# Optimization experiments

Measured on AMD Instinct MI355X. Metric: run time of the kernel, lower is better.

## Reference

```python
import jax, jax.numpy as jnp
import numpy as np

INPUT, HIDDEN, OUTPUT = 512, 1024, 512
B, T = 64, 512


def setup_inputs() -> dict:
    key = jax.random.key(0)
    ks = jax.random.split(key, 10)
    s_ih = (2.0 / (INPUT + HIDDEN)) ** 0.5
    s_hh = (2.0 / (INPUT + HIDDEN)) ** 0.5
    s_hy = (2.0 / (HIDDEN + OUTPUT)) ** 0.5
    inp = {
        "x": jax.random.normal(ks[0], (B, T, INPUT), dtype=jnp.float32),
        "W_xi": jax.random.normal(ks[1], (INPUT, HIDDEN), dtype=jnp.float32) * s_ih,
        "W_hi": jax.random.normal(ks[2], (HIDDEN, HIDDEN), dtype=jnp.float32) * s_hh,
        "b_i": jnp.zeros((HIDDEN,), dtype=jnp.float32),
        "W_xf": jax.random.normal(ks[3], (INPUT, HIDDEN), dtype=jnp.float32) * s_ih,
        "W_hf": jax.random.normal(ks[4], (HIDDEN, HIDDEN), dtype=jnp.float32) * s_hh,
        "b_f": jnp.zeros((HIDDEN,), dtype=jnp.float32),
        "W_xo": jax.random.normal(ks[5], (INPUT, HIDDEN), dtype=jnp.float32) * s_ih,
        "W_ho": jax.random.normal(ks[6], (HIDDEN, HIDDEN), dtype=jnp.float32) * s_hh,
        "b_o": jnp.zeros((HIDDEN,), dtype=jnp.float32),
        "W_xc": jax.random.normal(ks[7], (INPUT, HIDDEN), dtype=jnp.float32) * s_ih,
        "W_hc": jax.random.normal(ks[8], (HIDDEN, HIDDEN), dtype=jnp.float32) * s_hh,
        "b_c": jnp.zeros((HIDDEN,), dtype=jnp.float32),
        "W_hy": jax.random.normal(ks[9], (HIDDEN, OUTPUT), dtype=jnp.float32) * s_hy,
        "b_y": jnp.zeros((OUTPUT,), dtype=jnp.float32),
    }
    return inp


def reference(x, W_xi, W_hi, b_i, W_xf, W_hf, b_f, W_xo, W_ho, b_o,
              W_xc, W_hc, b_c, W_hy, b_y):
    Bn, Tn, _ = x.shape
    H = W_hi.shape[0]
    # Precompute input projections for all timesteps (one big GEMM per gate).
    xi = jnp.einsum('bti,ih->bth', x, W_xi) + b_i  # [B,T,H]
    xf = jnp.einsum('bti,ih->bth', x, W_xf) + b_f
    xo = jnp.einsum('bti,ih->bth', x, W_xo) + b_o
    xc = jnp.einsum('bti,ih->bth', x, W_xc) + b_c
    # time-major for scan
    xs = (jnp.swapaxes(xi, 0, 1), jnp.swapaxes(xf, 0, 1),
          jnp.swapaxes(xo, 0, 1), jnp.swapaxes(xc, 0, 1))

    def step(carry, xt):
        h, c = carry
        xi_t, xf_t, xo_t, xc_t = xt
        i_t = jax.nn.sigmoid(xi_t + h @ W_hi)
        f_t = jax.nn.sigmoid(xf_t + h @ W_hf)
        o_t = jax.nn.sigmoid(xo_t + h @ W_ho)
        cand = jnp.tanh(xc_t + h @ W_hc)
        c = f_t * c + i_t * cand
        h = o_t * jnp.tanh(c)
        return (h, c), h

    h0 = jnp.zeros((Bn, H), dtype=x.dtype)
    c0 = jnp.zeros((Bn, H), dtype=x.dtype)
    _, hs = jax.lax.scan(step, (h0, c0), xs)  # hs: [T,B,H]
    # Output projection applied to every step's hidden state.
    ys = jnp.einsum('tbh,ho->tbo', hs, W_hy) + b_y
    return jnp.swapaxes(ys, 0, 1)  # [B,T,O]
```

## Files before the change

### kernel.cpp

```cpp
#include <hip/hip_runtime.h>
#include <hip/hip_bf16.h>
#include <cstdint>

#define B_   64
#define T_   512
#define IN_  512
#define H_   1024
#define O_   512
#define NG   4096
#define KC   1536
#define BT   32768
#define BH   65536
#define NWG  128

using bs8 = __attribute__((ext_vector_type(8))) short;
using f4  = __attribute__((ext_vector_type(4))) float;

__device__ __forceinline__ ushort f2bf(float f) {
    union { float f; uint32_t u; } v; v.f = f;
    uint32_t r = v.u + 0x7fffu + ((v.u >> 16) & 1u);
    return (ushort)(r >> 16);
}
__device__ __forceinline__ float sigm(float x) { return 1.f / (1.f + __expf(-x)); }
__device__ __forceinline__ float tanh_(float x) {
    x = fminf(fmaxf(x, -15.f), 15.f);
    float e = __expf(2.f * x);
    return (e - 1.f) / (e + 1.f);
}
__device__ __forceinline__ void coh_store16(void* p, f4 v) {
    asm volatile("global_store_dwordx4 %0, %1, off sc0 sc1" :: "v"(p), "v"(v) : "memory");
}


__global__ void k_pack_x(const float* __restrict__ x, ushort* __restrict__ xP) {
    const int n8 = BT * IN_ / 8;
    for (int i = blockIdx.x * blockDim.x + threadIdx.x; i < n8; i += gridDim.x * blockDim.x) {
        const int e8 = i & 3, b = (i >> 2) & 63, kk = (i >> 8) & 15, t = i >> 12;
        const float* s = x + ((size_t)b * T_ + t) * IN_ + kk * 32 + e8 * 8;
        f4 v0 = *reinterpret_cast<const f4*>(s);
        f4 v1 = *reinterpret_cast<const f4*>(s + 4);
        uint4 q;
        q.x = (uint32_t)f2bf(v0[0]) | ((uint32_t)f2bf(v0[1]) << 16);
        q.y = (uint32_t)f2bf(v0[2]) | ((uint32_t)f2bf(v0[3]) << 16);
        q.z = (uint32_t)f2bf(v1[0]) | ((uint32_t)f2bf(v1[1]) << 16);
        q.w = (uint32_t)f2bf(v1[2]) | ((uint32_t)f2bf(v1[3]) << 16);
        *reinterpret_cast<uint4*>(xP + ((size_t)t * 16 + kk) * 2048 + b * 32 + e8 * 8) = q;
    }
}

__global__ void k_build_wcT(const float* __restrict__ xi, const float* __restrict__ xf,
                            const float* __restrict__ xo, const float* __restrict__ xc,
                            const float* __restrict__ hi, const float* __restrict__ hf,
                            const float* __restrict__ ho, const float* __restrict__ hc,
                            ushort* __restrict__ dst) {
    const int total = NG * KC;
    for (int i = blockIdx.x * blockDim.x + threadIdx.x; i < total; i += gridDim.x * blockDim.x) {
        int n = i / KC, k = i - n * KC;
        int g = n & 3, h = n >> 2;
        float v;
        if (k < IN_) {
            const float* s = (g == 0) ? xi : ((g == 1) ? xf : ((g == 2) ? xo : xc));
            v = s[(size_t)k * H_ + h];
        } else {
            const float* s = (g == 0) ? hi : ((g == 1) ? hf : ((g == 2) ? ho : hc));
            v = s[(size_t)(k - IN_) * H_ + h];
        }
        dst[i] = f2bf(v);
    }
}

__global__ void k_build_whyT(const float* __restrict__ w, ushort* __restrict__ dst) {
    const int total = O_ * H_;
    for (int i = blockIdx.x * blockDim.x + threadIdx.x; i < total; i += gridDim.x * blockDim.x) {
        int o = i >> 10, k = i & (H_ - 1);
        dst[i] = f2bf(w[(size_t)k * O_ + o]);
    }
}

__global__ void k_build_bias(const float* __restrict__ bi, const float* __restrict__ bff,
                             const float* __restrict__ bo, const float* __restrict__ bc,
                             float* __restrict__ dst) {
    int i = blockIdx.x * blockDim.x + threadIdx.x;
    if (i < NG) {
        int g = i & 3, h = i >> 2;
        dst[i] = (g == 0) ? bi[h] : ((g == 1) ? bff[h] : ((g == 2) ? bo[h] : bc[h]));
    }
}

#define WROWB 3072
#define WSWZ(row, kbyte) ((row) * WROWB + ((kbyte) ^ (((row) & 7) << 4)))

__global__ void __launch_bounds__(256, 1)
k_persist(const ushort* __restrict__ WcT, const ushort* __restrict__ xP,
          ushort* __restrict__ hs, float* __restrict__ cst,
          const float* __restrict__ biasc, uint32_t* __restrict__ flags,
          int t0, int nsteps) {
    __shared__ ushort Wl[32 * 1536];
    __shared__ ushort hout[64][8];
    const int g = blockIdx.x, tid = threadIdx.x;
    const int lane = tid & 63, w = tid >> 6;
    const int n0 = g * 32;
    const int l15 = lane & 15, lq = lane >> 4;

    {
        char* p = (char*)Wl;
        for (int i = tid; i < 32 * 192; i += 256) {
            const int row = i / 192, c8 = i - row * 192;
            bs8 v = *reinterpret_cast<const bs8*>(WcT + (size_t)(n0 + row) * KC + c8 * 8);
            *reinterpret_cast<bs8*>(p + WSWZ(row, c8 * 16)) = v;
        }
    }
    const char* wl = (const char*)Wl;

    const int bmy = w * 16 + l15;
    const int u0 = g * 8;
    const f4 bia0 = *reinterpret_cast<const f4*>(biasc + n0 + lq * 4);
    const f4 bia1 = *reinterpret_cast<const f4*>(biasc + n0 + 16 + lq * 4);
    float c0 = 0.f, c1 = 0.f;
    if (t0 != 0) {
        c0 = cst[(size_t)bmy * H_ + u0 + lq];
        c1 = cst[(size_t)bmy * H_ + u0 + 4 + lq];
    }
    const ushort* xbase = xP + (size_t)t0 * 32768 + (size_t)bmy * 32 + lq * 8;
    const ushort* hrd   = hs + (size_t)bmy * 32 + lq * 8;
    __syncthreads();

    bs8 xv[16];
#pragma unroll
    for (int kk = 0; kk < 16; ++kk)
        xv[kk] = *reinterpret_cast<const bs8*>(xbase + kk * 2048);

    for (int s = 0; s < nsteps; ++s) {
        const ushort* hb = hrd + (size_t)s * BH;
        bs8 hv0[16], hv1[16];
#pragma unroll
        for (int kk = 0; kk < 16; ++kk)
            hv0[kk] = *reinterpret_cast<const bs8*>(hb + kk * 2048);

        f4 a0 = {0.f, 0.f, 0.f, 0.f}, a1 = {0.f, 0.f, 0.f, 0.f};
#pragma unroll
        for (int kk = 0; kk < 16; ++kk) {
            bs8 wa0 = *reinterpret_cast<const bs8*>(wl + WSWZ(l15,      kk * 64 + lq * 16));
            bs8 wa1 = *reinterpret_cast<const bs8*>(wl + WSWZ(16 + l15, kk * 64 + lq * 16));
            a0 = __builtin_amdgcn_mfma_f32_16x16x32_bf16(wa0, xv[kk], a0, 0, 0, 0);
            a1 = __builtin_amdgcn_mfma_f32_16x16x32_bf16(wa1, xv[kk], a1, 0, 0, 0);
        }
#pragma unroll
        for (int kk = 0; kk < 16; ++kk)
            hv1[kk] = *reinterpret_cast<const bs8*>(hb + (16 + kk) * 2048);
#pragma unroll
        for (int kk = 0; kk < 16; ++kk) {
            bs8 wa0 = *reinterpret_cast<const bs8*>(wl + WSWZ(l15,      1024 + kk * 64 + lq * 16));
            bs8 wa1 = *reinterpret_cast<const bs8*>(wl + WSWZ(16 + l15, 1024 + kk * 64 + lq * 16));
            a0 = __builtin_amdgcn_mfma_f32_16x16x32_bf16(wa0, hv0[kk], a0, 0, 0, 0);
            a1 = __builtin_amdgcn_mfma_f32_16x16x32_bf16(wa1, hv0[kk], a1, 0, 0, 0);
        }
#pragma unroll
        for (int kk = 0; kk < 16; ++kk) {
            bs8 wa0 = *reinterpret_cast<const bs8*>(wl + WSWZ(l15,      2048 + kk * 64 + lq * 16));
            bs8 wa1 = *reinterpret_cast<const bs8*>(wl + WSWZ(16 + l15, 2048 + kk * 64 + lq * 16));
            a0 = __builtin_amdgcn_mfma_f32_16x16x32_bf16(wa0, hv1[kk], a0, 0, 0, 0);
            a1 = __builtin_amdgcn_mfma_f32_16x16x32_bf16(wa1, hv1[kk], a1, 0, 0, 0);
        }

        {
            float pi = a0[0] + bia0[0], pf = a0[1] + bia0[1];
            float po = a0[2] + bia0[2], pc = a0[3] + bia0[3];
            float iv = sigm(pi), fv = sigm(pf), ov = sigm(po), cv = tanh_(pc);
            c0 = fv * c0 + iv * cv;
            hout[bmy][lq] = f2bf(ov * tanh_(c0));
        }
        {
            float pi = a1[0] + bia1[0], pf = a1[1] + bia1[1];
            float po = a1[2] + bia1[2], pc = a1[3] + bia1[3];
            float iv = sigm(pi), fv = sigm(pf), ov = sigm(po), cv = tanh_(pc);
            c1 = fv * c1 + iv * cv;
            hout[bmy][4 + lq] = f2bf(ov * tanh_(c1));
        }
        __syncthreads();

        if (w == 0) {
            f4 hv = *reinterpret_cast<f4*>(&hout[lane][0]);
            ushort* dst = hs + (size_t)(s + 1) * BH + (size_t)(g >> 2) * 2048
                        + (size_t)lane * 32 + (g & 3) * 8;
            coh_store16(dst, hv);
            asm volatile("s_waitcnt vmcnt(0)" ::: "memory");
            if (tid == 0)
                __hip_atomic_store(&flags[g], (uint32_t)(s + 1),
                                   __ATOMIC_RELAXED, __HIP_MEMORY_SCOPE_AGENT);
        }

        if (s + 1 < nsteps) {
#pragma unroll
            for (int kk = 0; kk < 16; ++kk)
                xv[kk] = *reinterpret_cast<const bs8*>(xbase + (size_t)(s + 1) * 32768 + kk * 2048);
            if (w == 0) {
                const uint32_t tgt = (uint32_t)(s + 1);
                for (;;) {
                    uint32_t f0 = __hip_atomic_load(&flags[lane], __ATOMIC_RELAXED,
                                                    __HIP_MEMORY_SCOPE_AGENT);
                    uint32_t f1 = __hip_atomic_load(&flags[64 + lane], __ATOMIC_RELAXED,
                                                    __HIP_MEMORY_SCOPE_AGENT);
                    if (__all((int)(f0 >= tgt && f1 >= tgt))) break;
                    __builtin_amdgcn_s_sleep(1);
                }
            }
            __syncthreads();
        }
    }

    cst[(size_t)bmy * H_ + u0 + lq]     = c0;
    cst[(size_t)bmy * H_ + u0 + 4 + lq] = c1;
}

__global__ void __launch_bounds__(64) k_yproj(const ushort* __restrict__ WhyT,
                                              const ushort* __restrict__ hsbase,
                                              const float* __restrict__ by,
                                              float* __restrict__ out, int t_off) {
    const int lane = threadIdx.x;
    const int tloc = blockIdx.x;
    const int o0 = blockIdx.y * 64;
    const int l15 = lane & 15, lq = lane >> 4, lk = lq * 8;
    const int t = t_off + tloc;

    const ushort* slot = hsbase + (size_t)(tloc + 1) * BH;
    const ushort* apm[4]; const ushort* bp[4];
#pragma unroll
    for (int m = 0; m < 4; ++m) apm[m] = WhyT + (size_t)(o0 + m * 16 + l15) * H_ + lk;
#pragma unroll
    for (int n = 0; n < 4; ++n) bp[n] = slot + (size_t)(n * 16 + l15) * 32 + lk;

    f4 acc[4][4] = {};
    for (int kk = 0; kk < 32; ++kk) {
        bs8 a[4], b[4];
#pragma unroll
        for (int m = 0; m < 4; ++m) a[m] = *reinterpret_cast<const bs8*>(apm[m] + kk * 32);
#pragma unroll
        for (int n = 0; n < 4; ++n) b[n] = *reinterpret_cast<const bs8*>(bp[n] + (size_t)kk * 2048);
#pragma unroll
        for (int m = 0; m < 4; ++m)
#pragma unroll
            for (int n = 0; n < 4; ++n)
                acc[m][n] = __builtin_amdgcn_mfma_f32_16x16x32_bf16(a[m], b[n], acc[m][n], 0, 0, 0);
    }

#pragma unroll
    for (int m = 0; m < 4; ++m) {
        const int ob = o0 + m * 16 + lq * 4;
        const f4 bb = *reinterpret_cast<const f4*>(by + ob);
#pragma unroll
        for (int n = 0; n < 4; ++n) {
            const int b_ = n * 16 + l15;
            f4 v = acc[m][n] + bb;
            *reinterpret_cast<f4*>(out + ((size_t)b_ * T_ + t) * O_ + ob) = v;
        }
    }
}


extern "C" void kernel_launch(void* const* d_in, const int* in_sizes, int n_in,
                              void* d_out, int out_size, void* d_ws, size_t ws_size,
                              hipStream_t stream) {
    const float* x   = (const float*)d_in[0];
    const float* wxi = (const float*)d_in[1];
    const float* whi = (const float*)d_in[2];
    const float* bi  = (const float*)d_in[3];
    const float* wxf = (const float*)d_in[4];
    const float* whf = (const float*)d_in[5];
    const float* bf_ = (const float*)d_in[6];
    const float* wxo = (const float*)d_in[7];
    const float* who = (const float*)d_in[8];
    const float* bo  = (const float*)d_in[9];
    const float* wxc = (const float*)d_in[10];
    const float* whc = (const float*)d_in[11];
    const float* bc  = (const float*)d_in[12];
    const float* why = (const float*)d_in[13];
    const float* by  = (const float*)d_in[14];
    float* out = (float*)d_out;

    uint8_t* w = (uint8_t*)d_ws;
    ushort*   xP    = (ushort*)  (w);
    ushort*   WcT   = (ushort*)  (w + 33554432);
    ushort*   WhyT  = (ushort*)  (w + 46137344);
    float*    biasc = (float*)   (w + 47185920);
    float*    cst   = (float*)   (w + 47202304);
    uint32_t* flags = (uint32_t*)(w + 47464448);
    ushort*   hs    = (ushort*)  (w + 47468544);
    const size_t NEED_A = 47468544 + (size_t)(T_ + 1) * BH * 2;
    const size_t NEED_B = 47468544 + (size_t)65 * BH * 2;
    if (ws_size < NEED_B) return;
    const bool fullhs = (ws_size >= NEED_A);

    k_pack_x<<<2048, 256, 0, stream>>>(x, xP);
    k_build_wcT<<<4096, 256, 0, stream>>>(wxi, wxf, wxo, wxc, whi, whf, who, whc, WcT);
    k_build_whyT<<<512, 256, 0, stream>>>(why, WhyT);
    k_build_bias<<<16, 256, 0, stream>>>(bi, bf_, bo, bc, biasc);

    hipMemsetAsync(cst, 0, (size_t)BH * 4, stream);
    hipMemsetAsync(hs,  0, (size_t)BH * 2, stream);

    const int nchunk = fullhs ? 1 : 8;
    const int steps  = fullhs ? T_ : 64;
    for (int c = 0; c < nchunk; ++c) {
        const int t0 = c * steps;
        hipMemsetAsync(flags, 0, NWG * 4, stream);
        const ushort* a0 = WcT; const ushort* a1 = xP; ushort* a2 = hs;
        float* a3 = cst; const float* a4 = biasc; uint32_t* a5 = flags;
        int a6 = t0, a7 = steps;
        void* args[8] = {&a0, &a1, &a2, &a3, &a4, &a5, &a6, &a7};
        hipError_t e = hipLaunchCooperativeKernel((const void*)k_persist,
                                                  dim3(NWG), dim3(256), args, 0, stream);
        if (e != hipSuccess) {
            k_persist<<<dim3(NWG), dim3(256), 0, stream>>>(WcT, xP, hs, cst, biasc,
                                                           flags, t0, steps);
        }
        if (!fullhs) {
            k_yproj<<<dim3(64, O_ / 64), 64, 0, stream>>>(WhyT, hs, by, out, t0);
            if (c != nchunk - 1)
                hipMemcpyAsync(hs, hs + (size_t)64 * BH, (size_t)BH * 2,
                               hipMemcpyDeviceToDevice, stream);
        }
    }
    if (fullhs)
        k_yproj<<<dim3(T_, O_ / 64), 64, 0, stream>>>(WhyT, hs, by, out, 0);
}
```

Baseline: 2.877 ms.

## Split persistent LSTM over 256 workgroups with register-resident weights and K-split reduction

Raises the persistent recurrent kernel from 128 to 256 workgroups, so each owns 16 gate columns (4 hidden units) instead of 32. Recurrent weights now sit in registers: each wave holds a quarter of the K dimension for all 64 batch rows, replacing the per-step LDS weight reads. Per-wave partial accumulators are reduced through shared memory before the gate math. The intent is to spread the per-step matmul over more CUs and cut per-step latency, at the cost of an extra LDS reduction, an extra barrier, and a grid-wide spin wait that now polls 256 flags.

Result: slower. 3.692 ms (+28.3%).

```diff
diff --git a/kernel.cpp b/kernel.cpp
--- a/kernel.cpp
+++ b/kernel.cpp
@@ -11,7 +11,7 @@
 #define KC   1536
 #define BT   32768
 #define BH   65536
-#define NWG  128
+#define NWG  256
 
 using bs8 = __attribute__((ext_vector_type(8))) short;
 using f4  = __attribute__((ext_vector_type(4))) float;
@@ -26,9 +26,6 @@
     x = fminf(fmaxf(x, -15.f), 15.f);
     float e = __expf(2.f * x);
     return (e - 1.f) / (e + 1.f);
-}
-__device__ __forceinline__ void coh_store16(void* p, f4 v) {
-    asm volatile("global_store_dwordx4 %0, %1, off sc0 sc1" :: "v"(p), "v"(v) : "memory");
 }
 
 
@@ -87,103 +84,81 @@
     }
 }
 
-#define WROWB 3072
-#define WSWZ(row, kbyte) ((row) * WROWB + ((kbyte) ^ (((row) & 7) << 4)))
-
 __global__ void __launch_bounds__(256, 1)
 k_persist(const ushort* __restrict__ WcT, const ushort* __restrict__ xP,
           ushort* __restrict__ hs, float* __restrict__ cst,
           const float* __restrict__ biasc, uint32_t* __restrict__ flags,
           int t0, int nsteps) {
-    __shared__ ushort Wl[32 * 1536];
-    __shared__ ushort hout[64][8];
+    __shared__ f4 part[4][4][64];
+    __shared__ ushort hout[64][4];
     const int g = blockIdx.x, tid = threadIdx.x;
     const int lane = tid & 63, w = tid >> 6;
-    const int n0 = g * 32;
+    const int n0 = g * 16;
     const int l15 = lane & 15, lq = lane >> 4;
 
-    {
-        char* p = (char*)Wl;
-        for (int i = tid; i < 32 * 192; i += 256) {
-            const int row = i / 192, c8 = i - row * 192;
-            bs8 v = *reinterpret_cast<const bs8*>(WcT + (size_t)(n0 + row) * KC + c8 * 8);
-            *reinterpret_cast<bs8*>(p + WSWZ(row, c8 * 16)) = v;
-        }
-    }
-    const char* wl = (const char*)Wl;
+    bs8 wf[12];
+#pragma unroll
+    for (int j = 0; j < 12; ++j) {
+        const int c = w + 4 * j;
+        wf[j] = *reinterpret_cast<const bs8*>(WcT + (size_t)(n0 + l15) * KC + c * 32 + lq * 8);
+    }
 
     const int bmy = w * 16 + l15;
-    const int u0 = g * 8;
-    const f4 bia0 = *reinterpret_cast<const f4*>(biasc + n0 + lq * 4);
-    const f4 bia1 = *reinterpret_cast<const f4*>(biasc + n0 + 16 + lq * 4);
-    float c0 = 0.f, c1 = 0.f;
-    if (t0 != 0) {
-        c0 = cst[(size_t)bmy * H_ + u0 + lq];
-        c1 = cst[(size_t)bmy * H_ + u0 + 4 + lq];
-    }
-    const ushort* xbase = xP + (size_t)t0 * 32768 + (size_t)bmy * 32 + lq * 8;
-    const ushort* hrd   = hs + (size_t)bmy * 32 + lq * 8;
-    __syncthreads();
+    const int u = g * 4 + lq;
+    const f4 bia = *reinterpret_cast<const f4*>(biasc + n0 + lq * 4);
+    float creg = (t0 == 0) ? 0.f : cst[(size_t)bmy * H_ + u];
+
+    const ushort* xb = xP + (size_t)l15 * 32 + lq * 8;
+    const ushort* hb = hs + (size_t)l15 * 32 + lq * 8;
 
     bs8 xv[16];
 #pragma unroll
-    for (int kk = 0; kk < 16; ++kk)
-        xv[kk] = *reinterpret_cast<const bs8*>(xbase + kk * 2048);
+    for (int j = 0; j < 4; ++j)
+#pragma unroll
+        for (int bt = 0; bt < 4; ++bt)
+            xv[j * 4 + bt] = *reinterpret_cast<const bs8*>(
+                xb + ((size_t)t0 * 16 + (w + 4 * j)) * 2048 + bt * 512);
 
     for (int s = 0; s < nsteps; ++s) {
-        const ushort* hb = hrd + (size_t)s * BH;
-        bs8 hv0[16], hv1[16];
-#pragma unroll
-        for (int kk = 0; kk < 16; ++kk)
-            hv0[kk] = *reinterpret_cast<const bs8*>(hb + kk * 2048);
-
-        f4 a0 = {0.f, 0.f, 0.f, 0.f}, a1 = {0.f, 0.f, 0.f, 0.f};
-#pragma unroll
-        for (int kk = 0; kk < 16; ++kk) {
-            bs8 wa0 = *reinterpret_cast<const bs8*>(wl + WSWZ(l15,      kk * 64 + lq * 16));
-            bs8 wa1 = *reinterpret_cast<const bs8*>(wl + WSWZ(16 + l15, kk * 64 + lq * 16));
-            a0 = __builtin_amdgcn_mfma_f32_16x16x32_bf16(wa0, xv[kk], a0, 0, 0, 0);
-            a1 = __builtin_amdgcn_mfma_f32_16x16x32_bf16(wa1, xv[kk], a1, 0, 0, 0);
-        }
-#pragma unroll
-        for (int kk = 0; kk < 16; ++kk)
-            hv1[kk] = *reinterpret_cast<const bs8*>(hb + (16 + kk) * 2048);
-#pragma unroll
-        for (int kk = 0; kk < 16; ++kk) {
-            bs8 wa0 = *reinterpret_cast<const bs8*>(wl + WSWZ(l15,      1024 + kk * 64 + lq * 16));
-            bs8 wa1 = *reinterpret_cast<const bs8*>(wl + WSWZ(16 + l15, 1024 + kk * 64 + lq * 16));
-            a0 = __builtin_amdgcn_mfma_f32_16x16x32_bf16(wa0, hv0[kk], a0, 0, 0, 0);
-            a1 = __builtin_amdgcn_mfma_f32_16x16x32_bf16(wa1, hv0[kk], a1, 0, 0, 0);
-        }
-#pragma unroll
-        for (int kk = 0; kk < 16; ++kk) {
-            bs8 wa0 = *reinterpret_cast<const bs8*>(wl + WSWZ(l15,      2048 + kk * 64 + lq * 16));
-            bs8 wa1 = *reinterpret_cast<const bs8*>(wl + WSWZ(16 + l15, 2048 + kk * 64 + lq * 16));
-            a0 = __builtin_amdgcn_mfma_f32_16x16x32_bf16(wa0, hv1[kk], a0, 0, 0, 0);
-            a1 = __builtin_amdgcn_mfma_f32_16x16x32_bf16(wa1, hv1[kk], a1, 0, 0, 0);
-        }
-
-        {
-            float pi = a0[0] + bia0[0], pf = a0[1] + bia0[1];
-            float po = a0[2] + bia0[2], pc = a0[3] + bia0[3];
-            float iv = sigm(pi), fv = sigm(pf), ov = sigm(po), cv = tanh_(pc);
-            c0 = fv * c0 + iv * cv;
-            hout[bmy][lq] = f2bf(ov * tanh_(c0));
-        }
-        {
-            float pi = a1[0] + bia1[0], pf = a1[1] + bia1[1];
-            float po = a1[2] + bia1[2], pc = a1[3] + bia1[3];
-            float iv = sigm(pi), fv = sigm(pf), ov = sigm(po), cv = tanh_(pc);
-            c1 = fv * c1 + iv * cv;
-            hout[bmy][4 + lq] = f2bf(ov * tanh_(c1));
-        }
+        const ushort* hsl = hb + (size_t)s * BH;
+        bs8 hv[32];
+#pragma unroll
+        for (int j = 0; j < 8; ++j)
+#pragma unroll
+            for (int bt = 0; bt < 4; ++bt)
+                hv[j * 4 + bt] = *reinterpret_cast<const bs8*>(
+                    hsl + (size_t)(w + 4 * j) * 2048 + bt * 512);
+
+        f4 acc[4] = {{0.f,0.f,0.f,0.f},{0.f,0.f,0.f,0.f},{0.f,0.f,0.f,0.f},{0.f,0.f,0.f,0.f}};
+#pragma unroll
+        for (int j = 0; j < 4; ++j)
+#pragma unroll
+            for (int bt = 0; bt < 4; ++bt)
+                acc[bt] = __builtin_amdgcn_mfma_f32_16x16x32_bf16(wf[j], xv[j * 4 + bt], acc[bt], 0, 0, 0);
+
+#pragma unroll
+        for (int j = 0; j < 8; ++j)
+#pragma unroll
+            for (int bt = 0; bt < 4; ++bt)
+                acc[bt] = __builtin_amdgcn_mfma_f32_16x16x32_bf16(wf[4 + j], hv[j * 4 + bt], acc[bt], 0, 0, 0);
+
+#pragma unroll
+        for (int bt = 0; bt < 4; ++bt) part[w][bt][lane] = acc[bt];
         __syncthreads();
 
+        f4 ssum = part[0][w][lane] + part[1][w][lane] + part[2][w][lane] + part[3][w][lane];
+        float pi = ssum[0] + bia[0], pf = ssum[1] + bia[1];
+        float po = ssum[2] + bia[2], pc = ssum[3] + bia[3];
+        float iv = sigm(pi), fv = sigm(pf), ov = sigm(po), cv = tanh_(pc);
+        creg = fv * creg + iv * cv;
+        hout[bmy][lq] = f2bf(ov * tanh_(creg));
+        __syncthreads();
+
         if (w == 0) {
-            f4 hv = *reinterpret_cast<f4*>(&hout[lane][0]);
-            ushort* dst = hs + (size_t)(s + 1) * BH + (size_t)(g >> 2) * 2048
-                        + (size_t)lane * 32 + (g & 3) * 8;
-            coh_store16(dst, hv);
+            uint2 hv2 = *reinterpret_cast<uint2*>(&hout[lane][0]);
+            ushort* dst = hs + (size_t)(s + 1) * BH + (size_t)(g >> 3) * 2048
+                        + (size_t)lane * 32 + (g & 7) * 4;
+            asm volatile("global_store_dwordx2 %0, %1, off sc0 sc1" :: "v"(dst), "v"(hv2) : "memory");
             asm volatile("s_waitcnt vmcnt(0)" ::: "memory");
             if (tid == 0)
                 __hip_atomic_store(&flags[g], (uint32_t)(s + 1),
@@ -192,16 +167,19 @@
 
         if (s + 1 < nsteps) {
 #pragma unroll
-            for (int kk = 0; kk < 16; ++kk)
-                xv[kk] = *reinterpret_cast<const bs8*>(xbase + (size_t)(s + 1) * 32768 + kk * 2048);
+            for (int j = 0; j < 4; ++j)
+#pragma unroll
+                for (int bt = 0; bt < 4; ++bt)
+                    xv[j * 4 + bt] = *reinterpret_cast<const bs8*>(
+                        xb + ((size_t)(t0 + s + 1) * 16 + (w + 4 * j)) * 2048 + bt * 512);
             if (w == 0) {
                 const uint32_t tgt = (uint32_t)(s + 1);
                 for (;;) {
-                    uint32_t f0 = __hip_atomic_load(&flags[lane], __ATOMIC_RELAXED,
-                                                    __HIP_MEMORY_SCOPE_AGENT);
-                    uint32_t f1 = __hip_atomic_load(&flags[64 + lane], __ATOMIC_RELAXED,
-                                                    __HIP_MEMORY_SCOPE_AGENT);
-                    if (__all((int)(f0 >= tgt && f1 >= tgt))) break;
+                    uint32_t f0 = __hip_atomic_load(&flags[lane],       __ATOMIC_RELAXED, __HIP_MEMORY_SCOPE_AGENT);
+                    uint32_t f1 = __hip_atomic_load(&flags[64 + lane],  __ATOMIC_RELAXED, __HIP_MEMORY_SCOPE_AGENT);
+                    uint32_t f2 = __hip_atomic_load(&flags[128 + lane], __ATOMIC_RELAXED, __HIP_MEMORY_SCOPE_AGENT);
+                    uint32_t f3 = __hip_atomic_load(&flags[192 + lane], __ATOMIC_RELAXED, __HIP_MEMORY_SCOPE_AGENT);
+                    if (__all((int)(f0 >= tgt && f1 >= tgt && f2 >= tgt && f3 >= tgt))) break;
                     __builtin_amdgcn_s_sleep(1);
                 }
             }
@@ -209,8 +187,7 @@
         }
     }
 
-    cst[(size_t)bmy * H_ + u0 + lq]     = c0;
-    cst[(size_t)bmy * H_ + u0 + 4 + lq] = c1;
+    cst[(size_t)bmy * H_ + u] = creg;
 }
 
 __global__ void __launch_bounds__(64) k_yproj(const ushort* __restrict__ WhyT,
```
